# Kernel optimization log

Measured on AMD Instinct MI355X. Metric: run time of the kernel, lower is better.

The kernel has to match this reference:

```python
import jax, jax.numpy as jnp
import numpy as np

B, LQ, LK, DK, DV = 16, 1024, 1024, 256, 256
NEG = -1e9


def setup_inputs() -> dict:
    key = jax.random.key(0)
    kq, kk, kv, kw, km = jax.random.split(key, 5)
    return {
        "query": jax.random.normal(kq, (B, LQ, DK), dtype=jnp.float32),
        "key": jax.random.normal(kk, (B, LK, DK), dtype=jnp.float32),
        "value": jax.random.normal(kv, (B, LK, DV), dtype=jnp.float32),
        "w": jax.random.normal(kw, (DK,), dtype=jnp.float32),  # Linear(d_k,1,bias=False) weight
        "mask": jax.random.randint(km, (B, LQ, LK), 0, 2, dtype=jnp.int32),
    }


def reference(query, key, value, w, mask):
    # Bahdanau additive score: alignment_layer(query[:, :, None] + key[:, None, :]).squeeze(-1)
    # Exact linear decomposition: W·(q+k) = W·q + W·k, avoiding the (Lq,Lk,d_k) intermediate.
    q_s = jnp.einsum("bqd,d->bq", query, w)  # [B, Lq]
    k_s = jnp.einsum("bkd,d->bk", key, w)    # [B, Lk]
    scores = q_s[:, :, None] + k_s[:, None, :]  # [B, Lq, Lk]
    scores = jnp.where(mask == 0, NEG, scores)
    p_attn = jax.nn.softmax(scores, axis=-1)
    return jnp.matmul(p_attn, value)  # [B, Lq, Dv]
```

## Files before the change

### kernel.cpp

```cpp
#include <hip/hip_runtime.h>
#include <math.h>


#define NB     16
#define NL     1024
#define ND     256
#define NBKT   128

__global__ __launch_bounds__(256)
void ksm_kernel(const float* __restrict__ key, const float* __restrict__ w,
                const int* __restrict__ mask,
                float* __restrict__ ks, unsigned short* __restrict__ bmtab) {
    int wid  = threadIdx.x >> 6;
    int lane = threadIdx.x & 63;
    int row  = blockIdx.x * 4 + wid;

    const float4* krow = (const float4*)(key + (size_t)row * ND);
    float4 kv = krow[lane];
    float4 wv = ((const float4*)w)[lane];
    const int4* mrow4 = (const int4*)(mask + (size_t)row * NL);
    int4 m0 = mrow4[lane], m1 = mrow4[lane + 64];
    int4 m2 = mrow4[lane + 128], m3 = mrow4[lane + 192];

    float p = kv.x * wv.x + kv.y * wv.y + kv.z * wv.z + kv.w * wv.w;
    #pragma unroll
    for (int off = 32; off > 0; off >>= 1)
        p += __shfl_xor(p, off, 64);

    unsigned int bits = 0;
    bits |= (m0.x != 0 ? 1u : 0u) << 0;  bits |= (m0.y != 0 ? 1u : 0u) << 1;
    bits |= (m0.z != 0 ? 1u : 0u) << 2;  bits |= (m0.w != 0 ? 1u : 0u) << 3;
    bits |= (m1.x != 0 ? 1u : 0u) << 4;  bits |= (m1.y != 0 ? 1u : 0u) << 5;
    bits |= (m1.z != 0 ? 1u : 0u) << 6;  bits |= (m1.w != 0 ? 1u : 0u) << 7;
    bits |= (m2.x != 0 ? 1u : 0u) << 8;  bits |= (m2.y != 0 ? 1u : 0u) << 9;
    bits |= (m2.z != 0 ? 1u : 0u) << 10; bits |= (m2.w != 0 ? 1u : 0u) << 11;
    bits |= (m3.x != 0 ? 1u : 0u) << 12; bits |= (m3.y != 0 ? 1u : 0u) << 13;
    bits |= (m3.z != 0 ? 1u : 0u) << 14; bits |= (m3.w != 0 ? 1u : 0u) << 15;

    bmtab[(size_t)row * 64 + lane] = (unsigned short)bits;
    if (lane == 0) ks[row] = p;
}

__global__ __launch_bounds__(256)
void select_kernel(const float* __restrict__ ks,
                   float2* __restrict__ pk, float* __restrict__ rem) {
    __shared__ float se[NL];
    __shared__ int   cnt[NBKT];
    __shared__ int   cur[NBKT];
    __shared__ float wred[4];
    __shared__ float csum[16];
    const int b    = blockIdx.x;
    const int t    = threadIdx.x;
    const int lane = t & 63;
    const int wid  = t >> 6;
    const float* ksb = ks + b * NL;

    if (t < NBKT) cnt[t] = 0;

    float v0 = ksb[t], v1 = ksb[t + 256], v2 = ksb[t + 512], v3 = ksb[t + 768];

    float mx = fmaxf(fmaxf(v0, v1), fmaxf(v2, v3));
    #pragma unroll
    for (int off = 32; off > 0; off >>= 1)
        mx = fmaxf(mx, __shfl_xor(mx, off, 64));
    if (lane == 0) wred[wid] = mx;
    __syncthreads();
    const float m = fmaxf(fmaxf(wred[0], wred[1]), fmaxf(wred[2], wred[3]));

    float e0 = __expf(v0 - m), e1 = __expf(v1 - m);
    float e2 = __expf(v2 - m), e3 = __expf(v3 - m);
    int b0 = (int)fminf(m - v0, (float)(NBKT - 1));
    int b1 = (int)fminf(m - v1, (float)(NBKT - 1));
    int b2 = (int)fminf(m - v2, (float)(NBKT - 1));
    int b3 = (int)fminf(m - v3, (float)(NBKT - 1));
    atomicAdd(&cnt[b0], 1); atomicAdd(&cnt[b1], 1);
    atomicAdd(&cnt[b2], 1); atomicAdd(&cnt[b3], 1);
    __syncthreads();

    if (wid == 0) {
        int a  = cnt[lane];
        int b2v = cnt[lane + 64];
        int sa = a, sb = b2v;
        #pragma unroll
        for (int d = 1; d < 64; d <<= 1) {
            int na = __shfl_up(sa, d, 64);
            int nb = __shfl_up(sb, d, 64);
            if (lane >= d) { sa += na; sb += nb; }
        }
        int tot = __shfl(sa, 63, 64);
        sb += tot;
        cur[lane]      = sa - a;
        cur[lane + 64] = sb - b2v;
    }
    __syncthreads();

    int p0 = atomicAdd(&cur[b0], 1);
    int p1 = atomicAdd(&cur[b1], 1);
    int p2 = atomicAdd(&cur[b2], 1);
    int p3 = atomicAdd(&cur[b3], 1);
    se[p0] = e0; pk[b * NL + p0] = make_float2(e0, __int_as_float(t));
    se[p1] = e1; pk[b * NL + p1] = make_float2(e1, __int_as_float(t + 256));
    se[p2] = e2; pk[b * NL + p2] = make_float2(e2, __int_as_float(t + 512));
    se[p3] = e3; pk[b * NL + p3] = make_float2(e3, __int_as_float(t + 768));
    __syncthreads();

    #pragma unroll
    for (int cc = 0; cc < 4; ++cc) {
        int chunk = wid * 4 + cc;
        float s = se[chunk * 64 + lane];
        #pragma unroll
        for (int off = 32; off > 0; off >>= 1)
            s += __shfl_xor(s, off, 64);
        if (lane == 0) csum[chunk] = s;
    }
    __syncthreads();

    if (t == 0) {
        float run = 0.0f;
        for (int c = 15; c >= 0; --c) {
            rem[b * NL + c * 64 + 63] = run;
            run += csum[c];
        }
    }
}

__global__ __launch_bounds__(512)
void attn_kernel(const float* __restrict__ value, const int* __restrict__ mask,
                 const float2* __restrict__ pk, const float* __restrict__ rem,
                 const unsigned short* __restrict__ bmtab,
                 float* __restrict__ out) {
    __shared__ float lds_V[64 * ND];

    const int wid  = threadIdx.x >> 6;
    const int lane = threadIdx.x & 63;
    const int row0 = blockIdx.x * 32 + wid * 4;
    const int b    = row0 >> 10;
    const int base = b << 10;

    const float4* vbase = (const float4*)(value + ((size_t)b << 10) * ND);
    const float2* pk_g  = pk + base;

    float2 p0 = pk_g[lane];
    int   k0  = __float_as_int(p0.y);
    float e0  = p0.x;
    int   e0i = __float_as_int(e0);

    const int L     = (k0 >> 2) & 63;
    const int shift = (k0 & 3) + ((k0 >> 8) << 2);

    unsigned short t0 = bmtab[(size_t)(row0 + 0) * 64 + L];
    unsigned short t1 = bmtab[(size_t)(row0 + 1) * 64 + L];
    unsigned short t2 = bmtab[(size_t)(row0 + 2) * 64 + L];
    unsigned short t3 = bmtab[(size_t)(row0 + 3) * 64 + L];

    #pragma unroll
    for (int j = 0; j < 8; ++j) {
        int s   = wid * 8 + j;
        int ksr = __builtin_amdgcn_readlane(k0, s);
        ((float4*)lds_V)[s * 64 + lane] = vbase[(size_t)ksr * 64 + lane];
    }

    bool mb0 = (t0 >> shift) & 1;
    bool mb1 = (t1 >> shift) & 1;
    bool mb2 = (t2 >> shift) & 1;
    bool mb3 = (t3 >> shift) & 1;
    unsigned long long bm0 = __ballot(mb0);
    unsigned long long bm1 = __ballot(mb1);
    unsigned long long bm2 = __ballot(mb2);
    unsigned long long bm3 = __ballot(mb3);

    auto zsum = [&](bool mb) -> float {
        float wz = mb ? e0 : 0.0f;
        #pragma unroll
        for (int off = 32; off > 0; off >>= 1)
            wz += __shfl_xor(wz, off, 64);
        return wz;
    };
    float z0 = zsum(mb0), z1 = zsum(mb1), z2 = zsum(mb2), z3 = zsum(mb3);

    __syncthreads();

    float4 acc0 = make_float4(0.f, 0.f, 0.f, 0.f);
    float4 acc1 = make_float4(0.f, 0.f, 0.f, 0.f);
    float4 acc2 = make_float4(0.f, 0.f, 0.f, 0.f);
    float4 acc3 = make_float4(0.f, 0.f, 0.f, 0.f);

    #pragma unroll 16
    for (int i = 0; i < 64; ++i) {
        float4 v = ((const float4*)lds_V)[i * 64 + lane];
        float ei = __int_as_float(__builtin_amdgcn_readlane(e0i, i));
        float w0 = ((bm0 >> i) & 1ull) ? ei : 0.0f;
        float w1 = ((bm1 >> i) & 1ull) ? ei : 0.0f;
        float w2 = ((bm2 >> i) & 1ull) ? ei : 0.0f;
        float w3 = ((bm3 >> i) & 1ull) ? ei : 0.0f;
        acc0.x += w0 * v.x; acc0.y += w0 * v.y; acc0.z += w0 * v.z; acc0.w += w0 * v.w;
        acc1.x += w1 * v.x; acc1.y += w1 * v.y; acc1.z += w1 * v.z; acc1.w += w1 * v.w;
        acc2.x += w2 * v.x; acc2.y += w2 * v.y; acc2.z += w2 * v.z; acc2.w += w2 * v.w;
        acc3.x += w3 * v.x; acc3.y += w3 * v.y; acc3.z += w3 * v.z; acc3.w += w3 * v.w;
    }

    const float remv = rem[base + 63];

    auto finish_row = [&](int r, float4 acc, float Z) {
        const int* mrow = mask + (size_t)(row0 + r) * NL;
        bool done = (remv <= 1e-5f * Z);
        for (int c = 1; c < 16 && !done; ++c) {
            float2 p = pk_g[c * 64 + lane];
            float e  = p.x;
            int   k  = __float_as_int(p.y);
            bool mb  = (mrow[k] != 0);
            float dz = mb ? e : 0.0f;
            #pragma unroll
            for (int off = 32; off > 0; off >>= 1)
                dz += __shfl_xor(dz, off, 64);
            unsigned long long bmx = __ballot(mb);
            int eI = __float_as_int(e);
            for (int i = 0; i < 64; ++i) {
                float ei = __int_as_float(__builtin_amdgcn_readlane(eI, i));
                int   ki = __builtin_amdgcn_readlane(k, i);
                float w  = ((bmx >> i) & 1ull) ? ei : 0.0f;
                float4 v = vbase[(size_t)ki * 64 + lane];
                acc.x += w * v.x; acc.y += w * v.y;
                acc.z += w * v.z; acc.w += w * v.w;
            }
            Z += dz;
            done = (rem[base + c * 64 + 63] <= 1e-5f * Z);
        }
        float4* orow = (float4*)(out + (size_t)(row0 + r) * ND);
        if (Z > 0.0f) {
            float inv = 1.0f / Z;
            orow[lane] = make_float4(acc.x * inv, acc.y * inv,
                                     acc.z * inv, acc.w * inv);
        } else {
            float4 s = make_float4(0.f, 0.f, 0.f, 0.f);
            for (int k = 0; k < NL; ++k) {
                float4 v = vbase[(size_t)k * 64 + lane];
                s.x += v.x; s.y += v.y; s.z += v.z; s.w += v.w;
            }
            const float inv = 1.0f / (float)NL;
            orow[lane] = make_float4(s.x * inv, s.y * inv, s.z * inv, s.w * inv);
        }
    };
    finish_row(0, acc0, z0);
    finish_row(1, acc1, z1);
    finish_row(2, acc2, z2);
    finish_row(3, acc3, z3);
}

extern "C" void kernel_launch(void* const* d_in, const int* in_sizes, int n_in,
                              void* d_out, int out_size, void* d_ws, size_t ws_size,
                              hipStream_t stream) {
    const float* key   = (const float*)d_in[1];
    const float* value = (const float*)d_in[2];
    const float* w     = (const float*)d_in[3];
    const int*   mask  = (const int*)d_in[4];
    float*       outp  = (float*)d_out;

    float*  ks  = (float*)d_ws;
    float2* pkb = (float2*)(ks + NB * NL);
    float*  rem = (float*)(pkb + NB * NL);
    unsigned short* bmtab =
        (unsigned short*)(rem + NB * NL);

    ksm_kernel   <<<NB * NL / 4, 256, 0, stream>>>(key, w, mask, ks, bmtab);
    select_kernel<<<NB, 256, 0, stream>>>(ks, pkb, rem);
    attn_kernel  <<<NB * NL / 32, 512, 0, stream>>>(value, mask, pkb, rem,
                                                    bmtab, outp);
}
```

Before: 161.1 us.

## Fuse per-batch key sort into attention kernel, recomputing selection per block in LDS

Removes the separate select_kernel, which ran only 16 blocks, and moves its max, bucket sort, exp and chunk-sum logic into the start of every attention block. The sorted (e, k) pairs live in LDS instead of global memory, and the remaining-mass suffix sums come from csum in shared memory. This drops one launch, a serial low-occupancy stage and the global round-trip for pk and rem. In exchange, each of the 512 attention blocks redoes the per-batch sort, and LDS use grows by 8 KB plus the small arrays.

```diff
diff --git a/kernel.cpp b/kernel.cpp
--- a/kernel.cpp
+++ b/kernel.cpp
@@ -41,44 +41,49 @@
     if (lane == 0) ks[row] = p;
 }
 
-__global__ __launch_bounds__(256)
-void select_kernel(const float* __restrict__ ks,
-                   float2* __restrict__ pk, float* __restrict__ rem) {
-    __shared__ float se[NL];
-    __shared__ int   cnt[NBKT];
-    __shared__ int   cur[NBKT];
-    __shared__ float wred[4];
-    __shared__ float csum[16];
-    const int b    = blockIdx.x;
+__global__ __launch_bounds__(512)
+void attn_kernel(const float* __restrict__ value, const int* __restrict__ mask,
+                 const float* __restrict__ ks,
+                 const unsigned short* __restrict__ bmtab,
+                 float* __restrict__ out) {
+    __shared__ float  lds_V[64 * ND];
+    __shared__ float2 pk_lds[NL];
+    __shared__ int    cnt[NBKT];
+    __shared__ int    cur[NBKT];
+    __shared__ float  wred[8];
+    __shared__ float  csum[16];
+
     const int t    = threadIdx.x;
+    const int wid  = t >> 6;
     const int lane = t & 63;
-    const int wid  = t >> 6;
-    const float* ksb = ks + b * NL;
+    const int row0 = blockIdx.x * 32 + wid * 4;
+    const int b    = row0 >> 10;
+
+    const float4* vbase = (const float4*)(value + ((size_t)b << 10) * ND);
+    const float*  ksb   = ks + b * NL;
 
     if (t < NBKT) cnt[t] = 0;
 
-    float v0 = ksb[t], v1 = ksb[t + 256], v2 = ksb[t + 512], v3 = ksb[t + 768];
-
-    float mx = fmaxf(fmaxf(v0, v1), fmaxf(v2, v3));
+    float v0 = ksb[t], v1 = ksb[t + 512];
+
+    float mx = fmaxf(v0, v1);
     #pragma unroll
     for (int off = 32; off > 0; off >>= 1)
         mx = fmaxf(mx, __shfl_xor(mx, off, 64));
     if (lane == 0) wred[wid] = mx;
     __syncthreads();
-    const float m = fmaxf(fmaxf(wred[0], wred[1]), fmaxf(wred[2], wred[3]));
-
-    float e0 = __expf(v0 - m), e1 = __expf(v1 - m);
-    float e2 = __expf(v2 - m), e3 = __expf(v3 - m);
+    float m = wred[0];
+    #pragma unroll
+    for (int j = 1; j < 8; ++j) m = fmaxf(m, wred[j]);
+
+    float e0v = __expf(v0 - m), e1v = __expf(v1 - m);
     int b0 = (int)fminf(m - v0, (float)(NBKT - 1));
     int b1 = (int)fminf(m - v1, (float)(NBKT - 1));
-    int b2 = (int)fminf(m - v2, (float)(NBKT - 1));
-    int b3 = (int)fminf(m - v3, (float)(NBKT - 1));
     atomicAdd(&cnt[b0], 1); atomicAdd(&cnt[b1], 1);
-    atomicAdd(&cnt[b2], 1); atomicAdd(&cnt[b3], 1);
     __syncthreads();
 
     if (wid == 0) {
-        int a  = cnt[lane];
+        int a   = cnt[lane];
         int b2v = cnt[lane + 64];
         int sa = a, sb = b2v;
         #pragma unroll
@@ -94,53 +99,23 @@
     }
     __syncthreads();
 
-    int p0 = atomicAdd(&cur[b0], 1);
-    int p1 = atomicAdd(&cur[b1], 1);
-    int p2 = atomicAdd(&cur[b2], 1);
-    int p3 = atomicAdd(&cur[b3], 1);
-    se[p0] = e0; pk[b * NL + p0] = make_float2(e0, __int_as_float(t));
-    se[p1] = e1; pk[b * NL + p1] = make_float2(e1, __int_as_float(t + 256));
-    se[p2] = e2; pk[b * NL + p2] = make_float2(e2, __int_as_float(t + 512));
-    se[p3] = e3; pk[b * NL + p3] = make_float2(e3, __int_as_float(t + 768));
-    __syncthreads();
-
-    #pragma unroll
-    for (int cc = 0; cc < 4; ++cc) {
-        int chunk = wid * 4 + cc;
-        float s = se[chunk * 64 + lane];
+    int p0i = atomicAdd(&cur[b0], 1);
+    int p1i = atomicAdd(&cur[b1], 1);
+    pk_lds[p0i] = make_float2(e0v, __int_as_float(t));
+    pk_lds[p1i] = make_float2(e1v, __int_as_float(t + 512));
+    __syncthreads();
+
+    #pragma unroll
+    for (int cc = 0; cc < 2; ++cc) {
+        int chunk = wid * 2 + cc;
+        float s = pk_lds[chunk * 64 + lane].x;
         #pragma unroll
         for (int off = 32; off > 0; off >>= 1)
             s += __shfl_xor(s, off, 64);
         if (lane == 0) csum[chunk] = s;
     }
-    __syncthreads();
-
-    if (t == 0) {
-        float run = 0.0f;
-        for (int c = 15; c >= 0; --c) {
-            rem[b * NL + c * 64 + 63] = run;
-            run += csum[c];
-        }
-    }
-}
-
-__global__ __launch_bounds__(512)
-void attn_kernel(const float* __restrict__ value, const int* __restrict__ mask,
-                 const float2* __restrict__ pk, const float* __restrict__ rem,
-                 const unsigned short* __restrict__ bmtab,
-                 float* __restrict__ out) {
-    __shared__ float lds_V[64 * ND];
-
-    const int wid  = threadIdx.x >> 6;
-    const int lane = threadIdx.x & 63;
-    const int row0 = blockIdx.x * 32 + wid * 4;
-    const int b    = row0 >> 10;
-    const int base = b << 10;
-
-    const float4* vbase = (const float4*)(value + ((size_t)b << 10) * ND);
-    const float2* pk_g  = pk + base;
-
-    float2 p0 = pk_g[lane];
+
+    float2 p0 = pk_lds[lane];
     int   k0  = __float_as_int(p0.y);
     float e0  = p0.x;
     int   e0i = __float_as_int(e0);
@@ -199,13 +174,16 @@
         acc3.x += w3 * v.x; acc3.y += w3 * v.y; acc3.z += w3 * v.z; acc3.w += w3 * v.w;
     }
 
-    const float remv = rem[base + 63];
+    float remA = 0.0f;
+    #pragma unroll
+    for (int j = 1; j < 16; ++j) remA += csum[j];
 
     auto finish_row = [&](int r, float4 acc, float Z) {
         const int* mrow = mask + (size_t)(row0 + r) * NL;
-        bool done = (remv <= 1e-5f * Z);
+        float rsuf = remA;
+        bool done = (rsuf <= 1e-5f * Z);
         for (int c = 1; c < 16 && !done; ++c) {
-            float2 p = pk_g[c * 64 + lane];
+            float2 p = pk_lds[c * 64 + lane];
             float e  = p.x;
             int   k  = __float_as_int(p.y);
             bool mb  = (mrow[k] != 0);
@@ -224,7 +202,8 @@
                 acc.z += w * v.z; acc.w += w * v.w;
             }
             Z += dz;
-            done = (rem[base + c * 64 + 63] <= 1e-5f * Z);
+            rsuf -= csum[c];
+            done = (rsuf <= 1e-5f * Z);
         }
         float4* orow = (float4*)(out + (size_t)(row0 + r) * ND);
         if (Z > 0.0f) {
@@ -256,14 +235,10 @@
     const int*   mask  = (const int*)d_in[4];
     float*       outp  = (float*)d_out;
 
-    float*  ks  = (float*)d_ws;
-    float2* pkb = (float2*)(ks + NB * NL);
-    float*  rem = (float*)(pkb + NB * NL);
+    float* ks = (float*)d_ws;
     unsigned short* bmtab =
-        (unsigned short*)(rem + NB * NL);
-
-    ksm_kernel   <<<NB * NL / 4, 256, 0, stream>>>(key, w, mask, ks, bmtab);
-    select_kernel<<<NB, 256, 0, stream>>>(ks, pkb, rem);
-    attn_kernel  <<<NB * NL / 32, 512, 0, stream>>>(value, mask, pkb, rem,
-                                                    bmtab, outp);
+        (unsigned short*)(ks + NB * NL);
+
+    ksm_kernel <<<NB * NL / 4, 256, 0, stream>>>(key, w, mask, ks, bmtab);
+    attn_kernel<<<NB * NL / 32, 512, 0, stream>>>(value, mask, ks, bmtab, outp);
 }
```

New measurement: 158.0 us. About the same (-2.0%).
